# Performance work log

Measured on AMD Instinct MI355X. Metric: run time of the kernel, lower is better.

Reference implementation:

```python
import jax, jax.numpy as jnp
import numpy as np

N_NODES = 100000
N_EDGES = 3200000
DIMS = [3, 64, 64, 64, 128, 1024, 512, 256, 2]  # per GCNemb.__init__


def setup_inputs() -> dict:
    key = jax.random.key(0)
    ks = jax.random.split(key, 2 + 2 * 8)
    x = jax.random.normal(ks[0], (N_NODES, DIMS[0]), dtype=jnp.float32)
    edge_index = jax.random.randint(ks[1], (2, N_EDGES), 0, N_NODES, dtype=jnp.int64)
    inp = {"x": x, "edge_index": edge_index}
    for i in range(8):
        scale = 1.0 / np.sqrt(DIMS[i])
        inp[f"W{i}"] = jax.random.normal(ks[2 + 2 * i], (DIMS[i], DIMS[i + 1]), dtype=jnp.float32) * scale
        inp[f"b{i}"] = jnp.zeros((DIMS[i + 1],), dtype=jnp.float32)
    return inp


def _gcn_norm(edge_index, n):
    # PyG GCNConv default: add self-loops, symmetric normalization.
    loop = jnp.arange(n, dtype=edge_index.dtype)
    row = jnp.concatenate([edge_index[0], loop])  # source
    col = jnp.concatenate([edge_index[1], loop])  # target
    deg = jax.ops.segment_sum(jnp.ones_like(col, dtype=jnp.float32), col, num_segments=n)
    dinv = jnp.where(deg > 0, jax.lax.rsqrt(deg), 0.0)
    norm = dinv[row] * dinv[col]  # [E+N]
    return row, col, norm


def _gcn_conv(x, W, b, row, col, norm, n):
    h = x @ W  # [N, out]
    agg = jax.ops.segment_sum(h[row] * norm[:, None], col, num_segments=n)
    return agg + b


def reference(x, edge_index, W0, b0, W1, b1, W2, b2, W3, b3, W4, b4, W5, b5, W6, b6, W7, b7):
    n = x.shape[0]
    row, col, norm = _gcn_norm(edge_index, n)
    Ws = [W0, W1, W2, W3, W4, W5, W6, W7]
    bs = [b0, b1, b2, b3, b4, b5, b6, b7]
    for i in range(7):
        x = jax.nn.relu(_gcn_conv(x, Ws[i], bs[i], row, col, norm, n))
    return _gcn_conv(x, Ws[7], bs[7], row, col, norm, n)
```

## Files before the change

### kernel.cpp

```cpp
#include <hip/hip_runtime.h>
#include <hip/hip_bf16.h>
#include <cstdint>
#include <cstddef>


#define TPB 256
#define SI 8
#define STILE (TPB * SI)

typedef short short8 __attribute__((ext_vector_type(8)));
typedef float f32x4 __attribute__((ext_vector_type(4)));

__device__ __forceinline__ float b2f(unsigned short u) {
    union { unsigned int i; float f; } c; c.i = ((unsigned int)u) << 16; return c.f;
}
__device__ __forceinline__ unsigned short f2b(float f) {
    __hip_bfloat16 h = __float2bfloat16(f);
    union { __hip_bfloat16 h; unsigned short u; } c; c.h = h; return c.u;
}

__device__ __forceinline__ void async_copy16(void* lds, const void* g) {
    __builtin_amdgcn_global_load_lds(
        (const __attribute__((address_space(1))) void*)g,
        (__attribute__((address_space(3))) void*)lds,
        16, 0, 0);
}


__global__ void count_deg_kernel(const int* __restrict__ col, int* __restrict__ deg,
                                 int E, int n) {
    int e = blockIdx.x * blockDim.x + threadIdx.x;
    if (e < E) {
        int c = col[e];
        if ((unsigned)c < (unsigned)n) atomicAdd(&deg[c], 1);
    }
}

__global__ __launch_bounds__(TPB) void scan_part1(const int* __restrict__ deg,
                                                  int* __restrict__ bsum, int n) {
    int t0 = blockIdx.x * STILE + threadIdx.x * SI;
    int s = 0;
#pragma unroll
    for (int j = 0; j < SI; j++) { int i = t0 + j; if (i < n) s += deg[i]; }
#pragma unroll
    for (int off = 32; off >= 1; off >>= 1) s += __shfl_xor(s, off);
    __shared__ int ws[TPB / 64];
    if ((threadIdx.x & 63) == 0) ws[threadIdx.x >> 6] = s;
    __syncthreads();
    if (threadIdx.x == 0) {
        int tot = 0;
        for (int i = 0; i < TPB / 64; i++) tot += ws[i];
        bsum[blockIdx.x] = tot;
    }
}

__global__ void scan_part2(int* __restrict__ bsum, int nb,
                           int* __restrict__ rowptr, int n) {
    __shared__ int sums[1024];
    int tid = threadIdx.x;
    int v = (tid < nb) ? bsum[tid] : 0;
    sums[tid] = v;
    __syncthreads();
    for (int off = 1; off < 1024; off <<= 1) {
        int t = (tid >= off) ? sums[tid - off] : 0;
        __syncthreads();
        sums[tid] += t;
        __syncthreads();
    }
    if (tid < nb) bsum[tid] = (tid == 0) ? 0 : sums[tid - 1];
    if (tid == 0) rowptr[n] = sums[1023];
}

__global__ __launch_bounds__(TPB) void scan_part3(const int* __restrict__ deg,
                                                  const int* __restrict__ bsum,
                                                  int* __restrict__ rowptr,
                                                  int* __restrict__ cursor,
                                                  float* __restrict__ dinv, int n) {
    int tid = threadIdx.x;
    int lane = tid & 63, wv = tid >> 6;
    int t0 = blockIdx.x * STILE + tid * SI;
    int v[SI]; int s = 0;
#pragma unroll
    for (int j = 0; j < SI; j++) { int i = t0 + j; v[j] = (i < n) ? deg[i] : 0; s += v[j]; }
    int sc = s;
#pragma unroll
    for (int off = 1; off < 64; off <<= 1) {
        int t = __shfl_up(sc, off);
        if (lane >= off) sc += t;
    }
    __shared__ int wtot[TPB / 64];
    if (lane == 63) wtot[wv] = sc;
    __syncthreads();
    int woff = 0;
    for (int i = 0; i < wv; i++) woff += wtot[i];
    int off0 = bsum[blockIdx.x] + woff + (sc - s);
#pragma unroll
    for (int j = 0; j < SI; j++) {
        int i = t0 + j;
        if (i < n) {
            rowptr[i] = off0; cursor[i] = off0;
            dinv[i] = 1.0f / sqrtf((float)(v[j] + 1));
        }
        off0 += v[j];
    }
}

__global__ void fill_csr_kernel(const int* __restrict__ row, const int* __restrict__ col,
                                const float* __restrict__ dinv,
                                int* __restrict__ cursor, int2* __restrict__ es,
                                int E, int n) {
    int e = blockIdx.x * blockDim.x + threadIdx.x;
    if (e < E) {
        int c = col[e];
        if ((unsigned)c < (unsigned)n) {
            int r = row[e];
            int pos = atomicAdd(&cursor[c], 1);
            if ((unsigned)pos < (unsigned)E) {
                es[pos] = make_int2(r, __float_as_int(dinv[r]));
            }
        }
    }
}

__global__ void convert_wt_kernel(const float* __restrict__ W, unsigned short* __restrict__ Wt,
                                  int K, int M) {
    int idx = blockIdx.x * blockDim.x + threadIdx.x;
    if (idx < K * M) {
        int k = idx / M, m = idx % M;
        Wt[(size_t)m * K + k] = f2b(W[idx]);
    }
}


template <int VEC> struct Pack;
template <> struct Pack<1> { using T = unsigned short; };
template <> struct Pack<2> { using T = unsigned int; };
template <> struct Pack<4> { using T = uint2; };

template <int VEC>
__global__ __launch_bounds__(TPB) void agg_win_kernel(
        const unsigned short* __restrict__ x, unsigned short* __restrict__ out,
        const int* __restrict__ rowptr, const int2* __restrict__ es,
        const float* __restrict__ dinv, const float* __restrict__ bias,
        int n, int d, int wb, int relu) {
    using P = typename Pack<VEC>::T;
    int wid  = (blockIdx.x * blockDim.x + threadIdx.x) >> 6;
    int lane = threadIdx.x & 63;
    if (wid >= n) return;
    int start = rowptr[wid], end = rowptr[wid + 1];
    float acc[4][VEC];
#pragma unroll
    for (int g = 0; g < 4; g++)
#pragma unroll
        for (int j = 0; j < VEC; j++) acc[g][j] = 0.f;
    const int fo = wb + lane * VEC;
    union U { P v; unsigned short u[VEC]; };

    for (int base = start; base < end; base += 64) {
        int idx = base + lane;
        int clamped = (idx < end) ? idx : (end - 1);
        int2 ev = es[clamped];
        int   sv = ev.x;
        float dv = (idx < end) ? __int_as_float(ev.y) : 0.f;
        int cnt = end - base; if (cnt > 64) cnt = 64;
        int j = 0;
        for (; j + 8 <= cnt; j += 8) {
            int s[8]; float e[8]; U l[8];
#pragma unroll
            for (int q = 0; q < 8; q++) { s[q] = __shfl(sv, j + q); e[q] = __shfl(dv, j + q); }
#pragma unroll
            for (int q = 0; q < 8; q++) l[q].v = *(const P*)(x + (size_t)s[q] * d + fo);
#pragma unroll
            for (int q = 0; q < 8; q++)
#pragma unroll
                for (int t = 0; t < VEC; t++)
                    acc[q & 3][t] = fmaf(e[q], b2f(l[q].u[t]), acc[q & 3][t]);
        }
        for (; j < cnt; j++) {
            int   s0 = __shfl(sv, j);
            float e0 = __shfl(dv, j);
            U l0; l0.v = *(const P*)(x + (size_t)s0 * d + fo);
#pragma unroll
            for (int t = 0; t < VEC; t++) acc[0][t] = fmaf(e0, b2f(l0.u[t]), acc[0][t]);
        }
    }

    float di = dinv[wid];
    U ls; ls.v = *(const P*)(x + (size_t)wid * d + fo);
    U st;
#pragma unroll
    for (int j = 0; j < VEC; j++) {
        float a = (acc[0][j] + acc[1][j]) + (acc[2][j] + acc[3][j]);
        float v = di * (a + di * b2f(ls.u[j]));
        if (bias) v += bias[fo + j];
        if (relu) v = fmaxf(v, 0.f);
        st.u[j] = f2b(v);
    }
    *(P*)(out + (size_t)wid * d + fo) = st.v;
}

__global__ __launch_bounds__(TPB) void agg_dot2_kernel(
        const unsigned short* __restrict__ x,
        const int* __restrict__ rowptr, const int2* __restrict__ es,
        const float* __restrict__ dinv, const float* __restrict__ bias6,
        const float* __restrict__ W7, float* __restrict__ pre, int n) {
    int wid  = (blockIdx.x * blockDim.x + threadIdx.x) >> 6;
    int lane = threadIdx.x & 63;
    if (wid >= n) return;
    int start = rowptr[wid], end = rowptr[wid + 1];
    float acc[4][4];
#pragma unroll
    for (int g = 0; g < 4; g++)
#pragma unroll
        for (int j = 0; j < 4; j++) acc[g][j] = 0.f;
    const int fo = lane * 4;
    union U { uint2 v; unsigned short u[4]; };

    for (int base = start; base < end; base += 64) {
        int idx = base + lane;
        int clamped = (idx < end) ? idx : (end - 1);
        int2 ev = es[clamped];
        int   sv = ev.x;
        float dv = (idx < end) ? __int_as_float(ev.y) : 0.f;
        int cnt = end - base; if (cnt > 64) cnt = 64;
        int j = 0;
        for (; j + 8 <= cnt; j += 8) {
            int s[8]; float e[8]; U l[8];
#pragma unroll
            for (int q = 0; q < 8; q++) { s[q] = __shfl(sv, j + q); e[q] = __shfl(dv, j + q); }
#pragma unroll
            for (int q = 0; q < 8; q++) l[q].v = *(const uint2*)(x + (size_t)s[q] * 256 + fo);
#pragma unroll
            for (int q = 0; q < 8; q++)
#pragma unroll
                for (int t = 0; t < 4; t++)
                    acc[q & 3][t] = fmaf(e[q], b2f(l[q].u[t]), acc[q & 3][t]);
        }
        for (; j < cnt; j++) {
            int   s0 = __shfl(sv, j);
            float e0 = __shfl(dv, j);
            U l0; l0.v = *(const uint2*)(x + (size_t)s0 * 256 + fo);
#pragma unroll
            for (int t = 0; t < 4; t++) acc[0][t] = fmaf(e0, b2f(l0.u[t]), acc[0][t]);
        }
    }

    float di = dinv[wid];
    U ls; ls.v = *(const uint2*)(x + (size_t)wid * 256 + fo);
    float c0 = 0.f, c1 = 0.f;
#pragma unroll
    for (int j = 0; j < 4; j++) {
        float a = (acc[0][j] + acc[1][j]) + (acc[2][j] + acc[3][j]);
        float h = di * (a + di * b2f(ls.u[j])) + bias6[fo + j];
        h = fmaxf(h, 0.f);
        c0 = fmaf(h, W7[(fo + j) * 2 + 0], c0);
        c1 = fmaf(h, W7[(fo + j) * 2 + 1], c1);
    }
#pragma unroll
    for (int off = 32; off >= 1; off >>= 1) {
        c0 += __shfl_xor(c0, off);
        c1 += __shfl_xor(c1, off);
    }
    if (lane == 0) { pre[(size_t)wid * 2 + 0] = c0; pre[(size_t)wid * 2 + 1] = c1; }
}

__global__ __launch_bounds__(TPB) void agg_gemm64_kernel(
        const unsigned short* __restrict__ x, unsigned short* __restrict__ out,
        const int* __restrict__ rowptr, const int2* __restrict__ es,
        const float* __restrict__ dinv, const float* __restrict__ W,
        const float* __restrict__ bias, int n) {
    __shared__ float Ws[64 * 64];
    __shared__ float aggs[TPB / 64][64];
    const int tid = threadIdx.x;
    for (int i = tid; i < 64 * 64; i += TPB) Ws[i] = W[i];
    __syncthreads();
    int wid  = (blockIdx.x * TPB + tid) >> 6;
    int lane = tid & 63;
    int wv   = tid >> 6;
    if (wid >= n) return;
    int start = rowptr[wid], end = rowptr[wid + 1];
    float acc0 = 0.f, acc1 = 0.f, acc2 = 0.f, acc3 = 0.f;
    for (int base = start; base < end; base += 64) {
        int idx = base + lane;
        int clamped = (idx < end) ? idx : (end - 1);
        int2 ev = es[clamped];
        int   sv = ev.x;
        float dv = (idx < end) ? __int_as_float(ev.y) : 0.f;
        int cnt = end - base; if (cnt > 64) cnt = 64;
        int j = 0;
        for (; j + 4 <= cnt; j += 4) {
            int   s0 = __shfl(sv, j),     s1 = __shfl(sv, j + 1);
            int   s2 = __shfl(sv, j + 2), s3 = __shfl(sv, j + 3);
            float e0 = __shfl(dv, j),     e1 = __shfl(dv, j + 1);
            float e2 = __shfl(dv, j + 2), e3 = __shfl(dv, j + 3);
            acc0 = fmaf(e0, b2f(x[(size_t)s0 * 64 + lane]), acc0);
            acc1 = fmaf(e1, b2f(x[(size_t)s1 * 64 + lane]), acc1);
            acc2 = fmaf(e2, b2f(x[(size_t)s2 * 64 + lane]), acc2);
            acc3 = fmaf(e3, b2f(x[(size_t)s3 * 64 + lane]), acc3);
        }
        for (; j < cnt; j++) {
            int   s0 = __shfl(sv, j);
            float e0 = __shfl(dv, j);
            acc0 = fmaf(e0, b2f(x[(size_t)s0 * 64 + lane]), acc0);
        }
    }
    float di = dinv[wid];
    float a = di * (((acc0 + acc1) + (acc2 + acc3)) + di * b2f(x[(size_t)wid * 64 + lane]));
    aggs[wv][lane] = a;
    float v = bias[lane];
#pragma unroll 8
    for (int j = 0; j < 64; j++) v = fmaf(aggs[wv][j], Ws[j * 64 + lane], v);
    v = fmaxf(v, 0.f);
    out[(size_t)wid * 64 + lane] = f2b(v);
}

template <int D, int FUSE64>
__global__ __launch_bounds__(TPB) void agg_small_wave_kernel(
        const float* __restrict__ x, float* __restrict__ outf,
        unsigned short* __restrict__ outb,
        const int* __restrict__ rowptr, const int2* __restrict__ es,
        const float* __restrict__ dinv, const float* __restrict__ bias,
        const float* __restrict__ W, int n, int relu) {
    int wid  = (blockIdx.x * blockDim.x + threadIdx.x) >> 6;
    int lane = threadIdx.x & 63;
    if (wid >= n) return;
    int start = rowptr[wid], end = rowptr[wid + 1];
    float acc[D];
#pragma unroll
    for (int j = 0; j < D; j++) acc[j] = 0.f;
    for (int e = start + lane; e < end; e += 64) {
        int2 ev = es[e];
        int s = ev.x;
        float ds = __int_as_float(ev.y);
#pragma unroll
        for (int j = 0; j < D; j++) acc[j] = fmaf(ds, x[(size_t)s * D + j], acc[j]);
    }
#pragma unroll
    for (int j = 0; j < D; j++) {
#pragma unroll
        for (int off = 32; off >= 1; off >>= 1) acc[j] += __shfl_xor(acc[j], off);
    }
    float di = dinv[wid];
    float aggv[D];
#pragma unroll
    for (int j = 0; j < D; j++) aggv[j] = di * (acc[j] + di * x[(size_t)wid * D + j]);

    if (FUSE64) {
        float v = bias[lane];
#pragma unroll
        for (int j = 0; j < D; j++) v = fmaf(aggv[j], W[j * 64 + lane], v);
        v = fmaxf(v, 0.f);
        outb[(size_t)wid * 64 + lane] = f2b(v);
    } else {
        if (lane < D) {
            float v = aggv[lane];
            if (bias) v += bias[lane];
            if (relu) v = fmaxf(v, 0.f);
            outf[(size_t)wid * D + lane] = v;
        }
    }
}

__global__ __launch_bounds__(256) void gemm_mfma_kernel(
        const unsigned short* __restrict__ A, const unsigned short* __restrict__ Wt,
        const float* __restrict__ bias, unsigned short* __restrict__ C,
        int nr, int K, int M, int relu, int addbias) {
    __shared__ alignas(16) short As[128 * 32];
    __shared__ alignas(16) short Bs[128 * 32];
    const int tid  = threadIdx.x;
    const int w    = tid >> 6;
    const int lane = tid & 63;
    const int wr   = w >> 1;
    const int wc   = w & 1;
    const int row0 = blockIdx.x * 128;
    const int col0 = blockIdx.y * 128;

    f32x4 acc[4][4];
#pragma unroll
    for (int i = 0; i < 4; i++)
#pragma unroll
        for (int j = 0; j < 4; j++) acc[i][j] = {0.f, 0.f, 0.f, 0.f};

    const int lrow   = lane >> 2;
    const int lcolB  = (lane & 3) * 16;
    const int fm     = lane & 15;
    const int fq     = lane >> 4;

    for (int kk = 0; kk < K; kk += 32) {
#pragma unroll
        for (int i = 0; i < 2; i++) {
            int r = w * 32 + i * 16 + lrow;
            int grow = row0 + r;
            const char* g = (const char*)A + ((size_t)grow * K + kk) * 2 + lcolB;
            short* lds = &As[(w * 32 + i * 16) * 32];
            if (grow < nr) async_copy16(lds, g);
        }
#pragma unroll
        for (int i = 0; i < 2; i++) {
            int r = w * 32 + i * 16 + lrow;
            int gcol = col0 + r;
            const char* g = (const char*)Wt + ((size_t)gcol * K + kk) * 2 + lcolB;
            short* lds = &Bs[(w * 32 + i * 16) * 32];
            async_copy16(lds, g);
        }
        __syncthreads();

        short8 a[4], b[4];
#pragma unroll
        for (int i = 0; i < 4; i++) {
            a[i] = *(const short8*)&As[(wr * 64 + i * 16 + fm) * 32 + fq * 8];
            b[i] = *(const short8*)&Bs[(wc * 64 + i * 16 + fm) * 32 + fq * 8];
        }
#pragma unroll
        for (int mi = 0; mi < 4; mi++)
#pragma unroll
            for (int ni = 0; ni < 4; ni++)
                acc[mi][ni] = __builtin_amdgcn_mfma_f32_16x16x32_bf16(
                    a[mi], b[ni], acc[mi][ni], 0, 0, 0);
        __syncthreads();
    }

#pragma unroll
    for (int mi = 0; mi < 4; mi++) {
#pragma unroll
        for (int r = 0; r < 4; r++) {
            int row = row0 + wr * 64 + mi * 16 + fq * 4 + r;
            if (row >= nr) continue;
            size_t rb = (size_t)row * M;
#pragma unroll
            for (int ni = 0; ni < 4; ni++) {
                int col = col0 + wc * 64 + ni * 16 + fm;
                float v = acc[mi][ni][r];
                if (addbias) v += bias[col];
                if (relu) v = fmaxf(v, 0.f);
                C[rb + col] = f2b(v);
            }
        }
    }
}

static inline void launch_gemm_mfma(const unsigned short* A, const unsigned short* Wt,
                                    const float* bias, unsigned short* C,
                                    int nr, int K, int M, int relu, int addbias,
                                    hipStream_t stream) {
    dim3 grid((nr + 127) / 128, M / 128);
    gemm_mfma_kernel<<<grid, 256, 0, stream>>>(A, Wt, bias, C, nr, K, M, relu, addbias);
}


static inline size_t al256(size_t x) { return (x + 255) & ~(size_t)255; }

extern "C" void kernel_launch(void* const* d_in, const int* in_sizes, int n_in,
                              void* d_out, int out_size, void* d_ws, size_t ws_size,
                              hipStream_t stream) {
    const float* x  = (const float*)d_in[0];
    const int*   ei = (const int*)d_in[1];
    const int E = in_sizes[1] / 2;
    const int n = in_sizes[0] / 3;
    const int* rowv = ei;
    const int* colv = ei + E;

    const float* Wf[8]; const float* bt[8];
    for (int i = 0; i < 8; i++) { Wf[i] = (const float*)d_in[2 + 2 * i]; bt[i] = (const float*)d_in[3 + 2 * i]; }

    char* p = (char*)d_ws;
    size_t used = 0;
    auto carve = [&](size_t bytes) -> char* {
        char* r = p + used; used += al256(bytes); return r;
    };
    int*   deg    = (int*)carve((size_t)n * 4);
    float* dinv   = (float*)carve((size_t)n * 4);
    int*   rowptr = (int*)carve((size_t)(n + 1) * 4);
    int*   cursor = (int*)carve((size_t)(n + 1) * 4);
    int*   bsum   = (int*)carve(4096 * 4);
    int2*  es     = (int2*)carve((size_t)E * 8);
    unsigned short* bufA = (unsigned short*)carve((size_t)n * 512 * 2);
    unsigned short* bufB = (unsigned short*)carve((size_t)n * 512 * 2);
    const size_t wt3e = 64 * 128, wt4e = 128 * 1024, wt5e = 1024 * 512, wt6e = 512 * 256;
    unsigned short* wt3 = (unsigned short*)carve((wt3e + wt4e + wt5e + wt6e) * 2);
    unsigned short* wt4 = wt3 + wt3e;
    unsigned short* wt5 = wt4 + wt4e;
    unsigned short* wt6 = wt5 + wt5e;
    float* tmpf = (float*)carve((size_t)n * 2 * 4);

    size_t agg4_elems = al256((size_t)n * 128 * 2) / 2;
    unsigned short* tmpb = bufB + agg4_elems;
    size_t slack_elems = (size_t)n * 512 - agg4_elems;
    int chunk = (int)(slack_elems / 1024);
    if (chunk > n) chunk = n;
    chunk &= ~127;
    if (chunk < 128) chunk = 128;

    const int EB = (E + TPB - 1) / TPB;
    const int NW = (n + 3) / 4;
    const int SBK = (n + STILE - 1) / STILE;

    hipMemsetAsync(deg, 0, (size_t)n * 4, stream);
    count_deg_kernel<<<EB, TPB, 0, stream>>>(colv, deg, E, n);
    scan_part1<<<SBK, TPB, 0, stream>>>(deg, bsum, n);
    scan_part2<<<1, 1024, 0, stream>>>(bsum, SBK, rowptr, n);
    scan_part3<<<SBK, TPB, 0, stream>>>(deg, bsum, rowptr, cursor, dinv, n);
    fill_csr_kernel<<<EB, TPB, 0, stream>>>(rowv, colv, dinv, cursor, es, E, n);

    convert_wt_kernel<<<(int)((wt3e + 255) / 256), 256, 0, stream>>>(Wf[3], wt3, 64, 128);
    convert_wt_kernel<<<(int)((wt4e + 255) / 256), 256, 0, stream>>>(Wf[4], wt4, 128, 1024);
    convert_wt_kernel<<<(int)((wt5e + 255) / 256), 256, 0, stream>>>(Wf[5], wt5, 1024, 512);
    convert_wt_kernel<<<(int)((wt6e + 255) / 256), 256, 0, stream>>>(Wf[6], wt6, 512, 256);

    agg_small_wave_kernel<3, 1><<<NW, TPB, 0, stream>>>(
        x, nullptr, bufA, rowptr, es, dinv, bt[0], Wf[0], n, 1);

    agg_gemm64_kernel<<<NW, TPB, 0, stream>>>(bufA, bufB, rowptr, es, dinv, Wf[1], bt[1], n);
    agg_gemm64_kernel<<<NW, TPB, 0, stream>>>(bufB, bufA, rowptr, es, dinv, Wf[2], bt[2], n);

    agg_win_kernel<1><<<NW, TPB, 0, stream>>>(bufA, bufB, rowptr, es, dinv, nullptr, n, 64, 0, 0);
    launch_gemm_mfma(bufB, wt3, bt[3], bufA, n, 64, 128, 1, 1, stream);

    agg_win_kernel<2><<<NW, TPB, 0, stream>>>(bufA, bufB, rowptr, es, dinv, nullptr, n, 128, 0, 0);
    for (int r0 = 0; r0 < n; r0 += chunk) {
        int ch = n - r0; if (ch > chunk) ch = chunk;
        launch_gemm_mfma(bufB + (size_t)r0 * 128, wt4, bt[4], tmpb, ch, 128, 1024, 1, 1, stream);
        launch_gemm_mfma(tmpb, wt5, nullptr, bufA + (size_t)r0 * 512, ch, 1024, 512, 0, 0, stream);
    }
    agg_win_kernel<4><<<NW, TPB, 0, stream>>>(bufA, bufB, rowptr, es, dinv, bt[5], n, 512, 0, 1);
    agg_win_kernel<4><<<NW, TPB, 0, stream>>>(bufA, bufB, rowptr, es, dinv, bt[5], n, 512, 256, 1);

    launch_gemm_mfma(bufB, wt6, nullptr, bufA, n, 512, 256, 0, 0, stream);
    agg_dot2_kernel<<<NW, TPB, 0, stream>>>(bufA, rowptr, es, dinv, bt[6], Wf[7], tmpf, n);

    agg_small_wave_kernel<2, 0><<<NW, TPB, 0, stream>>>(
        tmpf, (float*)d_out, nullptr, rowptr, es, dinv, bt[7], nullptr, n, 0);
}
```

Baseline: 1.996 ms.

## Build CSR via two-pass bucketed scatter to localize per-node atomics

Replaces the single random-scatter CSR fill with a two-pass bucket sort. The first pass groups edges into 128-node buckets using a shared-memory histogram and block-level reservations, writing them into a staging buffer that reuses bufA. The second pass scatters each bucket with per-node atomics, which should now hit nearby memory. This is meant to cut the cost of random global atomics and scattered writes, but it adds an extra pass over the edges and extra staging traffic.

```diff
diff --git a/kernel.cpp b/kernel.cpp
--- a/kernel.cpp
+++ b/kernel.cpp
@@ -7,6 +7,9 @@
 #define TPB 256
 #define SI 8
 #define STILE (TPB * SI)
+#define BSH 7
+#define MAXBK 1024
+#define EPB 16384
 
 typedef short short8 __attribute__((ext_vector_type(8)));
 typedef float f32x4 __attribute__((ext_vector_type(4)));
@@ -102,6 +105,60 @@
             dinv[i] = 1.0f / sqrtf((float)(v[j] + 1));
         }
         off0 += v[j];
+    }
+}
+
+__global__ void bcur_init_kernel(const int* __restrict__ rowptr,
+                                 int* __restrict__ bcur, int nbk, int n) {
+    int b = blockIdx.x * blockDim.x + threadIdx.x;
+    if (b < nbk) {
+        int node = b << BSH; if (node > n) node = n;
+        bcur[b] = rowptr[node];
+    }
+}
+
+__global__ __launch_bounds__(TPB) void bucket_passA(
+        const int* __restrict__ row, const int* __restrict__ col,
+        int* __restrict__ bcur, int2* __restrict__ staging, int E, int n) {
+    __shared__ int hist[MAXBK];
+    __shared__ int base[MAXBK];
+    const int nbk = ((n + (1 << BSH) - 1) >> BSH);
+    const int tid = threadIdx.x;
+    for (int b = tid; b < nbk; b += TPB) hist[b] = 0;
+    __syncthreads();
+    int e0 = blockIdx.x * EPB;
+    int e1 = e0 + EPB; if (e1 > E) e1 = E;
+    for (int e = e0 + tid; e < e1; e += TPB) {
+        int c = col[e];
+        if ((unsigned)c < (unsigned)n) atomicAdd(&hist[c >> BSH], 1);
+    }
+    __syncthreads();
+    for (int b = tid; b < nbk; b += TPB) {
+        int h = hist[b];
+        base[b] = h ? atomicAdd(&bcur[b], h) : 0;
+        hist[b] = 0;
+    }
+    __syncthreads();
+    for (int e = e0 + tid; e < e1; e += TPB) {
+        int c = col[e];
+        if ((unsigned)c < (unsigned)n) {
+            int b = c >> BSH;
+            int slot = atomicAdd(&hist[b], 1);
+            staging[base[b] + slot] = make_int2(row[e], c);
+        }
+    }
+}
+
+__global__ void bucket_passB(const int2* __restrict__ staging,
+                             const float* __restrict__ dinv,
+                             int* __restrict__ cursor, int2* __restrict__ es,
+                             int E) {
+    int e = blockIdx.x * blockDim.x + threadIdx.x;
+    if (e < E) {
+        int2 t = staging[e];
+        int r = t.x, c = t.y;
+        int pos = atomicAdd(&cursor[c], 1);
+        es[pos] = make_int2(r, __float_as_int(dinv[r]));
     }
 }
 
@@ -483,6 +540,8 @@
     unsigned short* wt6 = wt5 + wt5e;
     float* tmpf = (float*)carve((size_t)n * 2 * 4);
 
+    int2* staging = (int2*)bufA;
+
     size_t agg4_elems = al256((size_t)n * 128 * 2) / 2;
     unsigned short* tmpb = bufB + agg4_elems;
     size_t slack_elems = (size_t)n * 512 - agg4_elems;
@@ -494,13 +553,20 @@
     const int EB = (E + TPB - 1) / TPB;
     const int NW = (n + 3) / 4;
     const int SBK = (n + STILE - 1) / STILE;
+    const int NBK = (n + (1 << BSH) - 1) >> BSH;
 
     hipMemsetAsync(deg, 0, (size_t)n * 4, stream);
     count_deg_kernel<<<EB, TPB, 0, stream>>>(colv, deg, E, n);
     scan_part1<<<SBK, TPB, 0, stream>>>(deg, bsum, n);
     scan_part2<<<1, 1024, 0, stream>>>(bsum, SBK, rowptr, n);
     scan_part3<<<SBK, TPB, 0, stream>>>(deg, bsum, rowptr, cursor, dinv, n);
-    fill_csr_kernel<<<EB, TPB, 0, stream>>>(rowv, colv, dinv, cursor, es, E, n);
+    if (NBK <= MAXBK) {
+        bcur_init_kernel<<<(NBK + 255) / 256, 256, 0, stream>>>(rowptr, bsum, NBK, n);
+        bucket_passA<<<(E + EPB - 1) / EPB, TPB, 0, stream>>>(rowv, colv, bsum, staging, E, n);
+        bucket_passB<<<EB, TPB, 0, stream>>>(staging, dinv, cursor, es, E);
+    } else {
+        fill_csr_kernel<<<EB, TPB, 0, stream>>>(rowv, colv, dinv, cursor, es, E, n);
+    }
 
     convert_wt_kernel<<<(int)((wt3e + 255) / 256), 256, 0, stream>>>(Wf[3], wt3, 64, 128);
     convert_wt_kernel<<<(int)((wt4e + 255) / 256), 256, 0, stream>>>(Wf[4], wt4, 128, 1024);
```

Result: no change. 1.995 ms (-0.0%).
